# Kernel tuning notes

Hardware: AMD Instinct MI355X
Metric: run time of the kernel (lower is better)

Reference implementation:

```python
import jax, jax.numpy as jnp
import numpy as np

B, C, H, W = 1, 512, 24, 24
N_HEADS, WS = 8, 7
PAD = WS // 2
HEAD_DIM = C // N_HEADS


def setup_inputs() -> dict:
    key = jax.random.key(0)
    ks = jax.random.split(key, 7)
    s = 0.02
    return {
        "x": jax.random.normal(ks[0], (B, C, H, W), dtype=jnp.float32),
        "Wq": s * jax.random.normal(ks[1], (C, C), dtype=jnp.float32),
        "bq": s * jax.random.normal(ks[2], (C,), dtype=jnp.float32),
        "Wk": s * jax.random.normal(ks[3], (C, C), dtype=jnp.float32),
        "bk": s * jax.random.normal(ks[4], (C,), dtype=jnp.float32),
        "Wv": s * jax.random.normal(ks[5], (C, C), dtype=jnp.float32),
        "bv": s * jax.random.normal(ks[6], (C,), dtype=jnp.float32),
        # module initializes gamma to zero; use small nonzero so output depends on attention
        "gamma": jnp.full((1,), 0.1, dtype=jnp.float32),
    }


def _conv1x1(z, Wt, bt):
    # 1x1 Conv2d == per-pixel GEMM over channels
    return jnp.einsum("bchw,oc->bohw", z, Wt) + bt[None, :, None, None]


def _windows(z):
    # z: (B, C, H+ws-1, W+ws-1) -> (B, n_heads, head_dim, ws*ws*H*W)
    # matches torch unfold(2,ws,1).unfold(3,ws,1).permute(0,1,4,5,2,3).view(...)
    taps = [z[:, :, di:di + H, dj:dj + W] for di in range(WS) for dj in range(WS)]
    w = jnp.stack(taps, axis=2)  # (B, C, ws*ws, H, W)
    return w.reshape(B, N_HEADS, HEAD_DIM, WS * WS * H * W)


def reference(x, Wq, bq, Wk, bk, Wv, bv, gamma):
    q = _conv1x1(x, Wq, bq).reshape(B, N_HEADS, HEAD_DIM, H * W)  # (B,h,d,HW)
    xp = jnp.pad(x, ((0, 0), (0, 0), (PAD, PAD), (PAD, PAD)), mode="reflect")
    k = _windows(_conv1x1(xp, Wk, bk))  # (B,h,d,ws^2*HW)
    v = _windows(_conv1x1(xp, Wv, bv))  # (B,h,d,ws^2*HW)
    # NOTE: as written in the source, each query attends to ALL ws^2*H*W keys
    energy = jnp.einsum("bhdq,bhdk->bhqk", q, k)  # (B,h,HW,ws^2*HW)
    attn = jax.nn.softmax(energy, axis=-1)
    out_w = jnp.einsum("bhqk,bhdk->bhdq", attn, v).reshape(B, C, H, W)
    return gamma * out_w + x
```

## Files before the change

### kernel.cpp

```cpp
#include <hip/hip_runtime.h>

#define HW   576
#define CC   512
#define PW   30
#define PPK  1024
#define NS   4
#define SP   256

typedef float f32x4 __attribute__((ext_vector_type(4)));
typedef short s16x8 __attribute__((ext_vector_type(8)));

__device__ __forceinline__ unsigned short f2bf(float f) {
    unsigned u = __float_as_uint(f);
    return (unsigned short)((u + 0x7FFFu + ((u >> 16) & 1u)) >> 16);
}
__device__ __forceinline__ float bf2f(unsigned short h) {
    return __uint_as_float((unsigned)h << 16);
}
__device__ __forceinline__ int smapf(int p) {
    if (p >= 900) return 576;
    const int y = p / PW, xw = p - y * PW;
    int iy = y - 3;  iy = (iy < 0) ? -iy : (iy > 23 ? 46 - iy : iy);
    int ix = xw - 3; ix = (ix < 0) ? -ix : (ix > 23 ? 46 - ix : ix);
    return iy * 24 + ix;
}

#define OFF_QT 0u
#define OFF_KT 589824u
#define OFF_VP 1638400u
#define OFF_MP 2686976u
#define OFF_LP 2760704u
#define OFF_OP 2834432u
#define OFF_XT 5193728u
#define OFF_WB 5784576u

__global__ __launch_bounds__(256) void cvtT(
    const float* __restrict__ x,
    const float* __restrict__ Wq, const float* __restrict__ Wk,
    const float* __restrict__ Wv,
    unsigned short* __restrict__ xT, unsigned short* __restrict__ wb)
{
    const int b = blockIdx.x, t = threadIdx.x;
    if (b < 72) {
        __shared__ float tile[64][65];
        const int pt = b % 9, ct = b / 9;
        const int p0 = pt * 64, c0 = ct * 64;
        const int tr = t >> 4, tc4 = (t & 15) * 4;
        #pragma unroll
        for (int cr = 0; cr < 4; ++cr) {
            const int row = cr * 16 + tr;
            const float4 v = *(const float4*)&x[(size_t)(c0 + row) * HW + p0 + tc4];
            tile[row][tc4 + 0] = v.x;
            tile[row][tc4 + 1] = v.y;
            tile[row][tc4 + 2] = v.z;
            tile[row][tc4 + 3] = v.w;
        }
        __syncthreads();
        #pragma unroll
        for (int cr = 0; cr < 4; ++cr) {
            const int prow = cr * 16 + tr;
            ushort4 o;
            o.x = f2bf(tile[tc4 + 0][prow]);
            o.y = f2bf(tile[tc4 + 1][prow]);
            o.z = f2bf(tile[tc4 + 2][prow]);
            o.w = f2bf(tile[tc4 + 3][prow]);
            *(ushort4*)&xT[(size_t)(p0 + prow) * CC + c0 + tc4] = o;
        }
    } else if (b == 72) {
        if (t < 128) *(ushort4*)&xT[(size_t)576 * CC + t * 4] = (ushort4){0, 0, 0, 0};
    } else {
        const int wi = (b - 73) * 2048 + t * 8;
        const int sel = wi >> 18, off = wi & 262143;
        const float* src = (sel == 0) ? Wq : (sel == 1) ? Wk : Wv;
        const float4 v0 = *(const float4*)&src[off];
        const float4 v1 = *(const float4*)&src[off + 4];
        ushort4 o0, o1;
        o0.x = f2bf(v0.x); o0.y = f2bf(v0.y); o0.z = f2bf(v0.z); o0.w = f2bf(v0.w);
        o1.x = f2bf(v1.x); o1.y = f2bf(v1.y); o1.z = f2bf(v1.z); o1.w = f2bf(v1.w);
        *(ushort4*)&wb[wi]     = o0;
        *(ushort4*)&wb[wi + 4] = o1;
    }
}

__global__ __launch_bounds__(256) void qkv_direct(
    const unsigned short* __restrict__ xT, const unsigned short* __restrict__ wb,
    const float* __restrict__ bq, const float* __restrict__ bk,
    const float* __restrict__ bv,
    unsigned short* __restrict__ qT, unsigned short* __restrict__ kT,
    unsigned short* __restrict__ vP)
{
    const int t = threadIdx.x;
    const int w = blockIdx.x * 4 + (t >> 6);
    const int lane = t & 63, fr = lane & 15, u = lane >> 4;

    int sel, m0, n0;
    if (w < 576)       { sel = 0; m0 = (w >> 4) << 4;               n0 = (w & 15) << 5; }
    else if (w < 1600) { const int k = w - 576;  sel = 1; m0 = (k >> 4) << 4; n0 = (k & 15) << 5; }
    else               { const int k = w - 1600; sel = 2; m0 = (k >> 5) << 4; n0 = (k & 31) << 5; }

    const unsigned short *A, *B;
    int ar, bn0, bn1;
    if (sel == 0)      { A = xT;          B = wb;          ar = m0 + fr;
                         bn0 = n0 + fr;          bn1 = n0 + 16 + fr; }
    else if (sel == 1) { A = xT;          B = wb + 262144; ar = smapf(m0 + fr);
                         bn0 = n0 + fr;          bn1 = n0 + 16 + fr; }
    else               { A = wb + 524288; B = xT;          ar = m0 + fr;
                         bn0 = smapf(n0 + fr);   bn1 = smapf(n0 + 16 + fr); }

    const unsigned short* Ap  = A + (size_t)ar  * CC + u * 8;
    const unsigned short* Bp0 = B + (size_t)bn0 * CC + u * 8;
    const unsigned short* Bp1 = B + (size_t)bn1 * CC + u * 8;

    f32x4 acc0 = (f32x4){0.f, 0.f, 0.f, 0.f};
    f32x4 acc1 = (f32x4){0.f, 0.f, 0.f, 0.f};
    #pragma unroll 8
    for (int k0 = 0; k0 < CC; k0 += 32) {
        const s16x8 a  = *(const s16x8*)(Ap  + k0);
        const s16x8 b0 = *(const s16x8*)(Bp0 + k0);
        const s16x8 b1 = *(const s16x8*)(Bp1 + k0);
        acc0 = __builtin_amdgcn_mfma_f32_16x16x32_bf16(a, b0, acc0, 0, 0, 0);
        acc1 = __builtin_amdgcn_mfma_f32_16x16x32_bf16(a, b1, acc1, 0, 0, 0);
    }

    #pragma unroll
    for (int ni = 0; ni < 2; ++ni) {
        const f32x4 acc = ni ? acc1 : acc0;
        #pragma unroll
        for (int r = 0; r < 4; ++r) {
            const int m = m0 + u * 4 + r;
            const int n = n0 + ni * 16 + fr;
            if (sel == 0) {
                qT[((size_t)(n >> 6) * HW + m) * 64 + (n & 63)] = f2bf(acc[r] + bq[n]);
            } else if (sel == 1) {
                kT[((size_t)(n >> 6) * PPK + m) * 64 + (n & 63)] = f2bf(acc[r] + bk[n]);
            } else {
                vP[((size_t)(m >> 6) * 64 + (m & 63)) * PPK + n] = f2bf(acc[r] + bv[m]);
            }
        }
    }
}

__global__ __launch_bounds__(256) void attn3(
    const unsigned short* __restrict__ qT, const unsigned short* __restrict__ kT,
    const unsigned short* __restrict__ vP, float* __restrict__ mP,
    float* __restrict__ lP, unsigned short* __restrict__ Op)
{
    const int q0 = blockIdx.x * 16;
    const int s  = blockIdx.y;
    const int hd = blockIdx.z;
    const int t  = threadIdx.x;
    const int lane = t & 63, w = t >> 6;
    const int fr = lane & 15, u = lane >> 4;

    __shared__ float cnt_s[SP];
    __shared__ __align__(16) unsigned short Wl[16 * 272];
    __shared__ float mw[64], lw[64];

    if (t < SP) {
        const int p = s * SP + t;
        float c = 0.f;
        if (p < 900) {
            const int y = p / PW, xw = p - y * PW;
            int cy = y + 1;  if (PW - y  < cy) cy = PW - y;  if (cy > 7) cy = 7;
            int cx = xw + 1; if (PW - xw < cx) cx = PW - xw; if (cx > 7) cx = 7;
            c = (float)(cy * cx);
        }
        cnt_s[t] = c;
    }

    const unsigned short* qrow = qT + ((size_t)hd * HW + q0 + fr) * 64 + u * 8;
    const s16x8 b0 = *(const s16x8*)qrow;
    const s16x8 b1 = *(const s16x8*)(qrow + 32);

    f32x4 e[4];
    #pragma unroll
    for (int t4 = 0; t4 < 4; ++t4) {
        const unsigned short* krow =
            kT + ((size_t)hd * PPK + s * SP + w * 64 + t4 * 16 + fr) * 64 + u * 8;
        const s16x8 a0 = *(const s16x8*)krow;
        const s16x8 a1 = *(const s16x8*)(krow + 32);
        f32x4 a = (f32x4){0.f, 0.f, 0.f, 0.f};
        a = __builtin_amdgcn_mfma_f32_16x16x32_bf16(a0, b0, a, 0, 0, 0);
        a = __builtin_amdgcn_mfma_f32_16x16x32_bf16(a1, b1, a, 0, 0, 0);
        e[t4] = a;
    }

    float m = -1e30f;
    #pragma unroll
    for (int t4 = 0; t4 < 4; ++t4)
        #pragma unroll
        for (int r = 0; r < 4; ++r) m = fmaxf(m, e[t4][r]);
    m = fmaxf(m, __shfl_xor(m, 16));
    m = fmaxf(m, __shfl_xor(m, 32));
    if (lane < 16) mw[w * 16 + lane] = m;
    __syncthreads();
    const float mq = fmaxf(fmaxf(mw[fr], mw[16 + fr]), fmaxf(mw[32 + fr], mw[48 + fr]));

    float sum = 0.f;
    #pragma unroll
    for (int t4 = 0; t4 < 4; ++t4) {
        unsigned short wb4[4];
        #pragma unroll
        for (int r = 0; r < 4; ++r) {
            const float wv2 = cnt_s[w * 64 + t4 * 16 + u * 4 + r] *
                              __expf(e[t4][r] - mq);
            sum += wv2;
            wb4[r] = f2bf(wv2);
        }
        const int ho = fr * 272 + w * 64 + t4 * 16 + u * 4;
        *(unsigned*)&Wl[ho]     = (unsigned)wb4[0] | ((unsigned)wb4[1] << 16);
        *(unsigned*)&Wl[ho + 2] = (unsigned)wb4[2] | ((unsigned)wb4[3] << 16);
    }
    sum += __shfl_xor(sum, 16);
    sum += __shfl_xor(sum, 32);
    if (lane < 16) lw[w * 16 + lane] = sum;
    __syncthreads();

    if (t < 16) {
        const float lq = lw[t] + lw[16 + t] + lw[32 + t] + lw[48 + t];
        const float mq2 = fmaxf(fmaxf(mw[t], mw[16 + t]),
                                fmaxf(mw[32 + t], mw[48 + t]));
        const int si = (hd * NS + s) * HW + q0 + t;
        lP[si] = lq;
        mP[si] = mq2;
    }

    f32x4 o = (f32x4){0.f, 0.f, 0.f, 0.f};
    const unsigned short* vrow =
        vP + ((size_t)hd * 64 + w * 16 + fr) * PPK + s * SP + u * 8;
    #pragma unroll
    for (int c = 0; c < 8; ++c) {
        const s16x8 aw = *(const s16x8*)&Wl[fr * 272 + c * 32 + u * 8];
        const s16x8 bv2 = *(const s16x8*)(vrow + c * 32);
        o = __builtin_amdgcn_mfma_f32_16x16x32_bf16(aw, bv2, o, 0, 0, 0);
    }
    #pragma unroll
    for (int r = 0; r < 4; ++r) {
        const size_t oi =
            ((size_t)(hd * NS + s) * HW + q0 + u * 4 + r) * 64 + w * 16 + fr;
        Op[oi] = f2bf(o[r]);
    }
}

__global__ __launch_bounds__(256) void combine2(
    const unsigned short* __restrict__ Op, const float* __restrict__ mP,
    const float* __restrict__ lP, const float* __restrict__ x,
    const float* __restrict__ gamma, float* __restrict__ out)
{
    const int hd = blockIdx.y;
    const int q  = blockIdx.x * 64 + (threadIdx.x >> 2);
    const int dq = (threadIdx.x & 3) * 16;

    const int sb = (hd * NS) * HW + q;
    const float m0 = mP[sb], m1 = mP[sb + HW];
    const float m2 = mP[sb + 2 * HW], m3 = mP[sb + 3 * HW];
    const float ms = fmaxf(fmaxf(m0, m1), fmaxf(m2, m3));
    const float a[NS] = {__expf(m0 - ms), __expf(m1 - ms),
                         __expf(m2 - ms), __expf(m3 - ms)};
    const float l = lP[sb] * a[0] + lP[sb + HW] * a[1] +
                    lP[sb + 2 * HW] * a[2] + lP[sb + 3 * HW] * a[3];
    const float scale = gamma[0] / l;

    float o[16] = {};
    #pragma unroll
    for (int s = 0; s < NS; ++s) {
        const unsigned short* op = &Op[((size_t)(sb + s * HW)) * 64 + dq];
        const uint4 u0 = *(const uint4*)op;
        const uint4 u1 = *(const uint4*)(op + 8);
        const unsigned uu[8] = {u0.x, u0.y, u0.z, u0.w, u1.x, u1.y, u1.z, u1.w};
        #pragma unroll
        for (int j = 0; j < 8; ++j) {
            o[2 * j]     = fmaf(a[s], bf2f((unsigned short)(uu[j] & 0xFFFF)), o[2 * j]);
            o[2 * j + 1] = fmaf(a[s], bf2f((unsigned short)(uu[j] >> 16)),    o[2 * j + 1]);
        }
    }
    #pragma unroll
    for (int i = 0; i < 16; ++i) {
        const size_t gi = (size_t)(hd * 64 + dq + i) * HW + q;
        out[gi] = fmaf(scale, o[i], x[gi]);
    }
}

extern "C" void kernel_launch(void* const* d_in, const int* in_sizes, int n_in,
                              void* d_out, int out_size, void* d_ws, size_t ws_size,
                              hipStream_t stream) {
    const float* x     = (const float*)d_in[0];
    const float* Wq    = (const float*)d_in[1];
    const float* bq    = (const float*)d_in[2];
    const float* Wk    = (const float*)d_in[3];
    const float* bk    = (const float*)d_in[4];
    const float* Wv    = (const float*)d_in[5];
    const float* bv    = (const float*)d_in[6];
    const float* gamma = (const float*)d_in[7];
    float* out = (float*)d_out;

    char* wsb = (char*)d_ws;
    unsigned short* qT = (unsigned short*)(wsb + OFF_QT);
    unsigned short* kT = (unsigned short*)(wsb + OFF_KT);
    unsigned short* vP = (unsigned short*)(wsb + OFF_VP);
    float*          mP = (float*)(wsb + OFF_MP);
    float*          lP = (float*)(wsb + OFF_LP);
    unsigned short* Op = (unsigned short*)(wsb + OFF_OP);
    unsigned short* xT = (unsigned short*)(wsb + OFF_XT);
    unsigned short* wb = (unsigned short*)(wsb + OFF_WB);

    cvtT<<<dim3(457), 256, 0, stream>>>(x, Wq, Wk, Wv, xT, wb);
    qkv_direct<<<dim3(656), 256, 0, stream>>>(xT, wb, bq, bk, bv, qT, kT, vP);
    attn3<<<dim3(36, NS, 8), 256, 0, stream>>>(qT, kT, vP, mP, lP, Op);
    combine2<<<dim3(9, 8), 256, 0, stream>>>(Op, mP, lP, x, gamma, out);
}
```

Baseline: 106.6 us.

## Fuse split-softmax combine into attention via last-block atomic counter

Removes the separate combine kernel launch. Each attention block bumps a per-(head, query-tile) counter once it has written its partial results, and the last of the four splits merges them. The merged tile goes through shared memory so the residual write to the output is coalesced. This trades one kernel launch and its tail for an atomic, thread fences and a serial merge in the last-arriving block. The counters are reset in the conversion kernel.

```diff
diff --git a/kernel.cpp b/kernel.cpp
--- a/kernel.cpp
+++ b/kernel.cpp
@@ -33,12 +33,14 @@
 #define OFF_OP 2834432u
 #define OFF_XT 5193728u
 #define OFF_WB 5784576u
+#define OFF_CNT 7357440u
 
 __global__ __launch_bounds__(256) void cvtT(
     const float* __restrict__ x,
     const float* __restrict__ Wq, const float* __restrict__ Wk,
     const float* __restrict__ Wv,
-    unsigned short* __restrict__ xT, unsigned short* __restrict__ wb)
+    unsigned short* __restrict__ xT, unsigned short* __restrict__ wb,
+    int* __restrict__ cnt)
 {
     const int b = blockIdx.x, t = threadIdx.x;
     if (b < 72) {
@@ -68,6 +70,7 @@
         }
     } else if (b == 72) {
         if (t < 128) *(ushort4*)&xT[(size_t)576 * CC + t * 4] = (ushort4){0, 0, 0, 0};
+        for (int i = t; i < 288; i += 256) cnt[i] = 0;
     } else {
         const int wi = (b - 73) * 2048 + t * 8;
         const int sel = wi >> 18, off = wi & 262143;
@@ -143,7 +146,9 @@
 __global__ __launch_bounds__(256) void attn3(
     const unsigned short* __restrict__ qT, const unsigned short* __restrict__ kT,
     const unsigned short* __restrict__ vP, float* __restrict__ mP,
-    float* __restrict__ lP, unsigned short* __restrict__ Op)
+    float* __restrict__ lP, unsigned short* __restrict__ Op,
+    const float* __restrict__ x, const float* __restrict__ gamma,
+    float* __restrict__ out, int* __restrict__ cnt)
 {
     const int q0 = blockIdx.x * 16;
     const int s  = blockIdx.y;
@@ -155,6 +160,7 @@
     __shared__ float cnt_s[SP];
     __shared__ __align__(16) unsigned short Wl[16 * 272];
     __shared__ float mw[64], lw[64];
+    __shared__ int lastf;
 
     if (t < SP) {
         const int p = s * SP + t;
@@ -240,44 +246,50 @@
             ((size_t)(hd * NS + s) * HW + q0 + u * 4 + r) * 64 + w * 16 + fr;
         Op[oi] = f2bf(o[r]);
     }
-}
-
-__global__ __launch_bounds__(256) void combine2(
-    const unsigned short* __restrict__ Op, const float* __restrict__ mP,
-    const float* __restrict__ lP, const float* __restrict__ x,
-    const float* __restrict__ gamma, float* __restrict__ out)
-{
-    const int hd = blockIdx.y;
-    const int q  = blockIdx.x * 64 + (threadIdx.x >> 2);
-    const int dq = (threadIdx.x & 3) * 16;
-
+
+    __syncthreads();
+    if (t == 0) {
+        __threadfence();
+        lastf = (atomicAdd(&cnt[hd * 36 + blockIdx.x], 1) == NS - 1);
+    }
+    __syncthreads();
+    if (!lastf) return;
+    __threadfence();
+
+    const int qA = t >> 4, dA = (t & 15) << 2;
+    const int q  = q0 + qA;
     const int sb = (hd * NS) * HW + q;
-    const float m0 = mP[sb], m1 = mP[sb + HW];
-    const float m2 = mP[sb + 2 * HW], m3 = mP[sb + 3 * HW];
-    const float ms = fmaxf(fmaxf(m0, m1), fmaxf(m2, m3));
-    const float a[NS] = {__expf(m0 - ms), __expf(m1 - ms),
-                         __expf(m2 - ms), __expf(m3 - ms)};
-    const float l = lP[sb] * a[0] + lP[sb + HW] * a[1] +
-                    lP[sb + 2 * HW] * a[2] + lP[sb + 3 * HW] * a[3];
-    const float scale = gamma[0] / l;
-
-    float o[16] = {};
-    #pragma unroll
-    for (int s = 0; s < NS; ++s) {
-        const unsigned short* op = &Op[((size_t)(sb + s * HW)) * 64 + dq];
-        const uint4 u0 = *(const uint4*)op;
-        const uint4 u1 = *(const uint4*)(op + 8);
-        const unsigned uu[8] = {u0.x, u0.y, u0.z, u0.w, u1.x, u1.y, u1.z, u1.w};
-        #pragma unroll
-        for (int j = 0; j < 8; ++j) {
-            o[2 * j]     = fmaf(a[s], bf2f((unsigned short)(uu[j] & 0xFFFF)), o[2 * j]);
-            o[2 * j + 1] = fmaf(a[s], bf2f((unsigned short)(uu[j] >> 16)),    o[2 * j + 1]);
-        }
-    }
-    #pragma unroll
-    for (int i = 0; i < 16; ++i) {
-        const size_t gi = (size_t)(hd * 64 + dq + i) * HW + q;
-        out[gi] = fmaf(scale, o[i], x[gi]);
+    const float m0_ = mP[sb], m1_ = mP[sb + HW];
+    const float m2_ = mP[sb + 2 * HW], m3_ = mP[sb + 3 * HW];
+    const float ms = fmaxf(fmaxf(m0_, m1_), fmaxf(m2_, m3_));
+    const float aa[NS] = {__expf(m0_ - ms), __expf(m1_ - ms),
+                          __expf(m2_ - ms), __expf(m3_ - ms)};
+    const float l = lP[sb] * aa[0] + lP[sb + HW] * aa[1] +
+                    lP[sb + 2 * HW] * aa[2] + lP[sb + 3 * HW] * aa[3];
+
+    float o4[4] = {0.f, 0.f, 0.f, 0.f};
+    #pragma unroll
+    for (int s2 = 0; s2 < NS; ++s2) {
+        const ushort4 uv = *(const ushort4*)&Op[((size_t)(hd * NS + s2) * HW + q) * 64 + dA];
+        o4[0] = fmaf(aa[s2], bf2f(uv.x), o4[0]);
+        o4[1] = fmaf(aa[s2], bf2f(uv.y), o4[1]);
+        o4[2] = fmaf(aa[s2], bf2f(uv.z), o4[2]);
+        o4[3] = fmaf(aa[s2], bf2f(uv.w), o4[3]);
+    }
+
+    float* Ol = (float*)Wl;
+    #pragma unroll
+    for (int j = 0; j < 4; ++j) Ol[(dA + j) * 17 + qA] = o4[j];
+    if ((t & 15) == 0) mw[qA] = gamma[0] / l;
+    __syncthreads();
+
+    const int qB = t & 15, d0 = (t >> 4) << 2;
+    const float sc = mw[qB];
+    #pragma unroll
+    for (int i = 0; i < 4; ++i) {
+        const int d = d0 + i;
+        const size_t gi = (size_t)(hd * 64 + d) * HW + q0 + qB;
+        out[gi] = fmaf(sc, Ol[d * 17 + qB], x[gi]);
     }
 }
 
@@ -303,9 +315,10 @@
     unsigned short* Op = (unsigned short*)(wsb + OFF_OP);
     unsigned short* xT = (unsigned short*)(wsb + OFF_XT);
     unsigned short* wb = (unsigned short*)(wsb + OFF_WB);
-
-    cvtT<<<dim3(457), 256, 0, stream>>>(x, Wq, Wk, Wv, xT, wb);
+    int*           cnt = (int*)(wsb + OFF_CNT);
+
+    cvtT<<<dim3(457), 256, 0, stream>>>(x, Wq, Wk, Wv, xT, wb, cnt);
     qkv_direct<<<dim3(656), 256, 0, stream>>>(xT, wb, bq, bk, bv, qT, kT, vP);
-    attn3<<<dim3(36, NS, 8), 256, 0, stream>>>(qT, kT, vP, mP, lP, Op);
-    combine2<<<dim3(9, 8), 256, 0, stream>>>(Op, mP, lP, x, gamma, out);
-}
+    attn3<<<dim3(36, NS, 8), 256, 0, stream>>>(qT, kT, vP, mP, lP, Op,
+                                               x, gamma, out, cnt);
+}
```

Result: slower. 180.9 us (+69.7%).

## Fuse split-key attention and combine into single full-key attention kernel

Applied to the files above, without the earlier changes.

Removes the 4-way key split and the separate combine kernel. Each block now processes all 1024 padded keys for a 16-query tile, does the softmax locally, and writes gamma-scaled output plus residual directly. This drops the partial O/m/l workspace traffic and one kernel launch. In exchange the grid shrinks from 1152 to 288 blocks, and each thread holds 16 energy accumulators with larger shared memory, which lowers parallelism and occupancy.

```diff
diff --git a/kernel.cpp b/kernel.cpp
--- a/kernel.cpp
+++ b/kernel.cpp
@@ -4,8 +4,6 @@
 #define CC   512
 #define PW   30
 #define PPK  1024
-#define NS   4
-#define SP   256
 
 typedef float f32x4 __attribute__((ext_vector_type(4)));
 typedef short s16x8 __attribute__((ext_vector_type(8)));
@@ -28,11 +26,8 @@
 #define OFF_QT 0u
 #define OFF_KT 589824u
 #define OFF_VP 1638400u
-#define OFF_MP 2686976u
-#define OFF_LP 2760704u
-#define OFF_OP 2834432u
-#define OFF_XT 5193728u
-#define OFF_WB 5784576u
+#define OFF_XT 2686976u
+#define OFF_WB 3277824u
 
 __global__ __launch_bounds__(256) void cvtT(
     const float* __restrict__ x,
@@ -140,43 +135,42 @@
     }
 }
 
-__global__ __launch_bounds__(256) void attn3(
+#define WLS 1040
+__global__ __launch_bounds__(256) void attn4(
     const unsigned short* __restrict__ qT, const unsigned short* __restrict__ kT,
-    const unsigned short* __restrict__ vP, float* __restrict__ mP,
-    float* __restrict__ lP, unsigned short* __restrict__ Op)
+    const unsigned short* __restrict__ vP, const float* __restrict__ x,
+    const float* __restrict__ gamma, float* __restrict__ out)
 {
     const int q0 = blockIdx.x * 16;
-    const int s  = blockIdx.y;
-    const int hd = blockIdx.z;
+    const int hd = blockIdx.y;
     const int t  = threadIdx.x;
     const int lane = t & 63, w = t >> 6;
     const int fr = lane & 15, u = lane >> 4;
 
-    __shared__ float cnt_s[SP];
-    __shared__ __align__(16) unsigned short Wl[16 * 272];
-    __shared__ float mw[64], lw[64];
-
-    if (t < SP) {
-        const int p = s * SP + t;
+    __shared__ float cnt_s[PPK];
+    __shared__ __align__(16) unsigned short Wl[16 * WLS];
+    __shared__ float mw[64], lw[64], sca[16];
+
+    for (int i = t; i < PPK; i += 256) {
         float c = 0.f;
-        if (p < 900) {
-            const int y = p / PW, xw = p - y * PW;
+        if (i < 900) {
+            const int y = i / PW, xw = i - y * PW;
             int cy = y + 1;  if (PW - y  < cy) cy = PW - y;  if (cy > 7) cy = 7;
             int cx = xw + 1; if (PW - xw < cx) cx = PW - xw; if (cx > 7) cx = 7;
             c = (float)(cy * cx);
         }
-        cnt_s[t] = c;
+        cnt_s[i] = c;
     }
 
     const unsigned short* qrow = qT + ((size_t)hd * HW + q0 + fr) * 64 + u * 8;
     const s16x8 b0 = *(const s16x8*)qrow;
     const s16x8 b1 = *(const s16x8*)(qrow + 32);
 
-    f32x4 e[4];
-    #pragma unroll
-    for (int t4 = 0; t4 < 4; ++t4) {
+    f32x4 e[16];
+    #pragma unroll
+    for (int t4 = 0; t4 < 16; ++t4) {
         const unsigned short* krow =
-            kT + ((size_t)hd * PPK + s * SP + w * 64 + t4 * 16 + fr) * 64 + u * 8;
+            kT + ((size_t)hd * PPK + w * 256 + t4 * 16 + fr) * 64 + u * 8;
         const s16x8 a0 = *(const s16x8*)krow;
         const s16x8 a1 = *(const s16x8*)(krow + 32);
         f32x4 a = (f32x4){0.f, 0.f, 0.f, 0.f};
@@ -187,7 +181,7 @@
 
     float m = -1e30f;
     #pragma unroll
-    for (int t4 = 0; t4 < 4; ++t4)
+    for (int t4 = 0; t4 < 16; ++t4)
         #pragma unroll
         for (int r = 0; r < 4; ++r) m = fmaxf(m, e[t4][r]);
     m = fmaxf(m, __shfl_xor(m, 16));
@@ -198,16 +192,17 @@
 
     float sum = 0.f;
     #pragma unroll
-    for (int t4 = 0; t4 < 4; ++t4) {
+    for (int t4 = 0; t4 < 16; ++t4) {
+        const float4 c4 = *(const float4*)&cnt_s[w * 256 + t4 * 16 + u * 4];
+        const float cw[4] = {c4.x, c4.y, c4.z, c4.w};
         unsigned short wb4[4];
         #pragma unroll
         for (int r = 0; r < 4; ++r) {
-            const float wv2 = cnt_s[w * 64 + t4 * 16 + u * 4 + r] *
-                              __expf(e[t4][r] - mq);
+            const float wv2 = cw[r] * __expf(e[t4][r] - mq);
             sum += wv2;
             wb4[r] = f2bf(wv2);
         }
-        const int ho = fr * 272 + w * 64 + t4 * 16 + u * 4;
+        const int ho = fr * WLS + w * 256 + t4 * 16 + u * 4;
         *(unsigned*)&Wl[ho]     = (unsigned)wb4[0] | ((unsigned)wb4[1] << 16);
         *(unsigned*)&Wl[ho + 2] = (unsigned)wb4[2] | ((unsigned)wb4[3] << 16);
     }
@@ -218,67 +213,29 @@
 
     if (t < 16) {
         const float lq = lw[t] + lw[16 + t] + lw[32 + t] + lw[48 + t];
-        const float mq2 = fmaxf(fmaxf(mw[t], mw[16 + t]),
-                                fmaxf(mw[32 + t], mw[48 + t]));
-        const int si = (hd * NS + s) * HW + q0 + t;
-        lP[si] = lq;
-        mP[si] = mq2;
+        sca[t] = gamma[0] / lq;
     }
 
     f32x4 o = (f32x4){0.f, 0.f, 0.f, 0.f};
     const unsigned short* vrow =
-        vP + ((size_t)hd * 64 + w * 16 + fr) * PPK + s * SP + u * 8;
-    #pragma unroll
-    for (int c = 0; c < 8; ++c) {
-        const s16x8 aw = *(const s16x8*)&Wl[fr * 272 + c * 32 + u * 8];
+        vP + ((size_t)hd * 64 + w * 16 + fr) * PPK + u * 8;
+    #pragma unroll 8
+    for (int c = 0; c < 32; ++c) {
+        const s16x8 aw = *(const s16x8*)&Wl[fr * WLS + c * 32 + u * 8];
         const s16x8 bv2 = *(const s16x8*)(vrow + c * 32);
         o = __builtin_amdgcn_mfma_f32_16x16x32_bf16(aw, bv2, o, 0, 0, 0);
     }
-    #pragma unroll
-    for (int r = 0; r < 4; ++r) {
-        const size_t oi =
-            ((size_t)(hd * NS + s) * HW + q0 + u * 4 + r) * 64 + w * 16 + fr;
-        Op[oi] = f2bf(o[r]);
-    }
-}
-
-__global__ __launch_bounds__(256) void combine2(
-    const unsigned short* __restrict__ Op, const float* __restrict__ mP,
-    const float* __restrict__ lP, const float* __restrict__ x,
-    const float* __restrict__ gamma, float* __restrict__ out)
-{
-    const int hd = blockIdx.y;
-    const int q  = blockIdx.x * 64 + (threadIdx.x >> 2);
-    const int dq = (threadIdx.x & 3) * 16;
-
-    const int sb = (hd * NS) * HW + q;
-    const float m0 = mP[sb], m1 = mP[sb + HW];
-    const float m2 = mP[sb + 2 * HW], m3 = mP[sb + 3 * HW];
-    const float ms = fmaxf(fmaxf(m0, m1), fmaxf(m2, m3));
-    const float a[NS] = {__expf(m0 - ms), __expf(m1 - ms),
-                         __expf(m2 - ms), __expf(m3 - ms)};
-    const float l = lP[sb] * a[0] + lP[sb + HW] * a[1] +
-                    lP[sb + 2 * HW] * a[2] + lP[sb + 3 * HW] * a[3];
-    const float scale = gamma[0] / l;
-
-    float o[16] = {};
-    #pragma unroll
-    for (int s = 0; s < NS; ++s) {
-        const unsigned short* op = &Op[((size_t)(sb + s * HW)) * 64 + dq];
-        const uint4 u0 = *(const uint4*)op;
-        const uint4 u1 = *(const uint4*)(op + 8);
-        const unsigned uu[8] = {u0.x, u0.y, u0.z, u0.w, u1.x, u1.y, u1.z, u1.w};
-        #pragma unroll
-        for (int j = 0; j < 8; ++j) {
-            o[2 * j]     = fmaf(a[s], bf2f((unsigned short)(uu[j] & 0xFFFF)), o[2 * j]);
-            o[2 * j + 1] = fmaf(a[s], bf2f((unsigned short)(uu[j] >> 16)),    o[2 * j + 1]);
-        }
-    }
-    #pragma unroll
-    for (int i = 0; i < 16; ++i) {
-        const size_t gi = (size_t)(hd * 64 + dq + i) * HW + q;
-        out[gi] = fmaf(scale, o[i], x[gi]);
-    }
+    __syncthreads();
+
+    const int d = hd * 64 + w * 16 + fr;
+    const size_t gb = (size_t)d * HW + q0 + u * 4;
+    const float4 x4 = *(const float4*)&x[gb];
+    float4 o4;
+    o4.x = fmaf(sca[u * 4 + 0], o[0], x4.x);
+    o4.y = fmaf(sca[u * 4 + 1], o[1], x4.y);
+    o4.z = fmaf(sca[u * 4 + 2], o[2], x4.z);
+    o4.w = fmaf(sca[u * 4 + 3], o[3], x4.w);
+    *(float4*)&out[gb] = o4;
 }
 
 extern "C" void kernel_launch(void* const* d_in, const int* in_sizes, int n_in,
@@ -298,14 +255,10 @@
     unsigned short* qT = (unsigned short*)(wsb + OFF_QT);
     unsigned short* kT = (unsigned short*)(wsb + OFF_KT);
     unsigned short* vP = (unsigned short*)(wsb + OFF_VP);
-    float*          mP = (float*)(wsb + OFF_MP);
-    float*          lP = (float*)(wsb + OFF_LP);
-    unsigned short* Op = (unsigned short*)(wsb + OFF_OP);
     unsigned short* xT = (unsigned short*)(wsb + OFF_XT);
     unsigned short* wb = (unsigned short*)(wsb + OFF_WB);
 
     cvtT<<<dim3(457), 256, 0, stream>>>(x, Wq, Wk, Wv, xT, wb);
     qkv_direct<<<dim3(656), 256, 0, stream>>>(xT, wb, bq, bk, bv, qT, kT, vP);
-    attn3<<<dim3(36, NS, 8), 256, 0, stream>>>(qT, kT, vP, mP, lP, Op);
-    combine2<<<dim3(9, 8), 256, 0, stream>>>(Op, mP, lP, x, gamma, out);
-}
+    attn4<<<dim3(36, 8), 256, 0, stream>>>(qT, kT, vP, x, gamma, out);
+}
```

New measurement: 109.0 us. 2.3% more time.
